# Performance work log

Measured on AMD Instinct MI355X. Metric: run time of the kernel, lower is better.

Reference implementation:

```python
import jax, jax.numpy as jnp
import numpy as np

N_NODES = 100000


def setup_inputs() -> dict:
    key = jax.random.key(0)
    ks = jax.random.split(key, 7)
    feats = jax.random.normal(ks[0], (N_NODES, 128), dtype=jnp.float32)
    src = jax.random.randint(ks[1], (1000000,), 0, N_NODES)
    dst = jax.random.randint(ks[2], (1000000,), 0, N_NODES)
    W1 = jax.random.normal(ks[3], (128, 128), dtype=jnp.float32) * (1.0 / np.sqrt(128))
    b1 = jnp.zeros((128,), dtype=jnp.float32)
    W2 = jax.random.normal(ks[4], (128, 40), dtype=jnp.float32) * (1.0 / np.sqrt(128))
    b2 = jnp.zeros((40,), dtype=jnp.float32)
    return {"feats": feats, "src": src, "dst": dst, "W1": W1, "b1": b1, "W2": W2, "b2": b2}


def _sage_gcn_layer(h, src, dst, deg, W, b):
    # DGL SAGEConv aggregator_type='gcn':
    #   neigh = sum over in-edges of src features; h = (neigh + h_self) / (in_deg + 1); out = h @ W + b
    neigh = jax.ops.segment_sum(h[src], dst, num_segments=N_NODES)  # [N, d]
    agg = (neigh + h) / (deg[:, None] + 1.0)
    return agg @ W + b


def reference(feats, src, dst, W1, b1, W2, b2):
    deg = jax.ops.segment_sum(jnp.ones_like(dst, dtype=feats.dtype), dst, num_segments=N_NODES)
    h1 = jax.nn.relu(_sage_gcn_layer(feats, src, dst, deg, W1, b1))  # dropout = identity (eval)
    h2 = _sage_gcn_layer(h1, src, dst, deg, W2, b2)
    # original returns (h_list, h); h_list = [h1, h2], final h = h2
    return (h1, h2)
```

## Files before the change

### kernel.cpp

```cpp
#include <hip/hip_runtime.h>

static inline int ceil_div(int a, int b){ return (a+b-1)/b; }

__global__ __launch_bounds__(256) void k_hist(const int* __restrict__ dst, int E, int* __restrict__ cnt){
  int e = blockIdx.x*256 + threadIdx.x;
  if (e < E) atomicAdd(&cnt[dst[e]], 1);
}

__global__ __launch_bounds__(256) void k_scan_a(const int* __restrict__ cnt, int N, int* __restrict__ bsum){
  __shared__ int s[256];
  int t = threadIdx.x;
  int i0 = blockIdx.x*512 + 2*t;
  int a = (i0   < N) ? cnt[i0]   : 0;
  int b = (i0+1 < N) ? cnt[i0+1] : 0;
  s[t] = a + b;
  __syncthreads();
  for (int off=128; off>0; off>>=1){ if (t<off) s[t]+=s[t+off]; __syncthreads(); }
  if (t==0) bsum[blockIdx.x] = s[0];
}

__global__ __launch_bounds__(256) void k_scan_b(int* __restrict__ bsum, int nb){
  __shared__ int s[256];
  int t = threadIdx.x;
  int v0=0,v1=0,v2=0,v3=0;
  int i0 = t*4;
  if (i0   < nb) v0 = bsum[i0];
  if (i0+1 < nb) v1 = bsum[i0+1];
  if (i0+2 < nb) v2 = bsum[i0+2];
  if (i0+3 < nb) v3 = bsum[i0+3];
  int tsum = v0+v1+v2+v3;
  s[t] = tsum;
  __syncthreads();
  for (int off=1; off<256; off<<=1){
    int v = (t>=off) ? s[t-off] : 0;
    __syncthreads();
    s[t] += v;
    __syncthreads();
  }
  int excl = s[t] - tsum;
  if (i0   < nb) bsum[i0]   = excl;
  if (i0+1 < nb) bsum[i0+1] = excl + v0;
  if (i0+2 < nb) bsum[i0+2] = excl + v0 + v1;
  if (i0+3 < nb) bsum[i0+3] = excl + v0 + v1 + v2;
}

__global__ __launch_bounds__(256) void k_scan_c(const int* __restrict__ cnt, int N,
                                                const int* __restrict__ bsum, int* __restrict__ offs){
  __shared__ int s[256];
  int t = threadIdx.x;
  int i0 = blockIdx.x*512 + 2*t;
  int a = (i0   < N) ? cnt[i0]   : 0;
  int b = (i0+1 < N) ? cnt[i0+1] : 0;
  int tsum = a+b;
  s[t] = tsum;
  __syncthreads();
  for (int off=1; off<256; off<<=1){
    int v = (t>=off) ? s[t-off] : 0;
    __syncthreads();
    s[t] += v;
    __syncthreads();
  }
  int excl = s[t] - tsum + bsum[blockIdx.x];
  if (i0   < N) offs[i0]   = excl;
  if (i0+1 < N) offs[i0+1] = excl + a;
}

__global__ __launch_bounds__(256) void k_place(const int* __restrict__ src, const int* __restrict__ dst, int E,
                                               int* __restrict__ offs, int* __restrict__ ss){
  int e = blockIdx.x*256 + threadIdx.x;
  if (e < E){
    int d = dst[e];
    int p = atomicAdd(&offs[d], 1);
    ss[p] = src[e];
  }
}

__global__ __launch_bounds__(256) void k_fused1(const float* __restrict__ feats,
    const int* __restrict__ ss, const int* __restrict__ offs, const int* __restrict__ cnt,
    const float* __restrict__ W1, const float* __restrict__ b1,
    const float* __restrict__ W2,
    float* __restrict__ h1, float* __restrict__ t1, int N){
  __shared__ float sA[64*132];
  __shared__ float sW[40*132];
  int t = threadIdx.x;
  int r0 = blockIdx.x*64;

  {
    int wid = t >> 6, lane = t & 63;
    const float2* f2 = (const float2*)feats;
    for (int k2=0; k2<16; ++k2){
      int rr = wid*16 + k2;
      int w  = r0 + rr;
      float2 acc = make_float2(0.f, 0.f);
      if (w < N){
        int c   = __builtin_amdgcn_readfirstlane(cnt[w]);
        int beg = __builtin_amdgcn_readfirstlane(offs[w]) - c;
        acc = f2[(size_t)w*64 + lane];
        int i = 0;
        for (; i+8 <= c; i += 8){
          int s0=ss[beg+i  ], s1=ss[beg+i+1], s2=ss[beg+i+2], s3=ss[beg+i+3];
          int s4=ss[beg+i+4], s5=ss[beg+i+5], s6=ss[beg+i+6], s7=ss[beg+i+7];
          float2 a0=f2[(size_t)s0*64+lane], a1=f2[(size_t)s1*64+lane];
          float2 a2=f2[(size_t)s2*64+lane], a3=f2[(size_t)s3*64+lane];
          float2 a4=f2[(size_t)s4*64+lane], a5=f2[(size_t)s5*64+lane];
          float2 a6=f2[(size_t)s6*64+lane], a7=f2[(size_t)s7*64+lane];
          acc.x += ((a0.x+a1.x)+(a2.x+a3.x)) + ((a4.x+a5.x)+(a6.x+a7.x));
          acc.y += ((a0.y+a1.y)+(a2.y+a3.y)) + ((a4.y+a5.y)+(a6.y+a7.y));
        }
        for (; i < c; ++i){
          int s0 = ss[beg+i];
          float2 a = f2[(size_t)s0*64 + lane];
          acc.x += a.x; acc.y += a.y;
        }
        float inv = 1.0f / (float)(c + 1);
        acc.x *= inv; acc.y *= inv;
      }
      *(float2*)&sA[rr*132 + 2*lane] = acc;
    }
  }

  int rg = t>>4, cg = t&15;
  float acc[4][8];
#pragma unroll
  for (int i=0;i<4;++i)
#pragma unroll
    for (int j=0;j<8;++j) acc[i][j]=0.f;

  for (int kc=0; kc<4; ++kc){
    __syncthreads();
#pragma unroll
    for (int it=0; it<4; ++it){
      int flat = it*1024 + t*4;
      *(float4*)&sW[flat] = *(const float4*)(W1 + kc*4096 + flat);
    }
    __syncthreads();
#pragma unroll 4
    for (int dd=0; dd<32; ++dd){
      int d = kc*32 + dd;
      float4 w0 = *(const float4*)&sW[dd*128 + cg*4];
      float4 w1 = *(const float4*)&sW[dd*128 + 64 + cg*4];
      float a0 = sA[(rg   )*132 + d];
      float a1 = sA[(rg+16)*132 + d];
      float a2 = sA[(rg+32)*132 + d];
      float a3 = sA[(rg+48)*132 + d];
      acc[0][0]+=a0*w0.x; acc[0][1]+=a0*w0.y; acc[0][2]+=a0*w0.z; acc[0][3]+=a0*w0.w;
      acc[0][4]+=a0*w1.x; acc[0][5]+=a0*w1.y; acc[0][6]+=a0*w1.z; acc[0][7]+=a0*w1.w;
      acc[1][0]+=a1*w0.x; acc[1][1]+=a1*w0.y; acc[1][2]+=a1*w0.z; acc[1][3]+=a1*w0.w;
      acc[1][4]+=a1*w1.x; acc[1][5]+=a1*w1.y; acc[1][6]+=a1*w1.z; acc[1][7]+=a1*w1.w;
      acc[2][0]+=a2*w0.x; acc[2][1]+=a2*w0.y; acc[2][2]+=a2*w0.z; acc[2][3]+=a2*w0.w;
      acc[2][4]+=a2*w1.x; acc[2][5]+=a2*w1.y; acc[2][6]+=a2*w1.z; acc[2][7]+=a2*w1.w;
      acc[3][0]+=a3*w0.x; acc[3][1]+=a3*w0.y; acc[3][2]+=a3*w0.z; acc[3][3]+=a3*w0.w;
      acc[3][4]+=a3*w1.x; acc[3][5]+=a3*w1.y; acc[3][6]+=a3*w1.z; acc[3][7]+=a3*w1.w;
    }
  }
  __syncthreads();

  float4 bb0 = *(const float4*)(b1 + cg*4);
  float4 bb1 = *(const float4*)(b1 + 64 + cg*4);
#pragma unroll
  for (int i=0;i<4;++i){
    int rr = rg + i*16;
    int r  = r0 + rr;
    float4 o0, o1;
    o0.x = fmaxf(acc[i][0]+bb0.x, 0.f); o0.y = fmaxf(acc[i][1]+bb0.y, 0.f);
    o0.z = fmaxf(acc[i][2]+bb0.z, 0.f); o0.w = fmaxf(acc[i][3]+bb0.w, 0.f);
    o1.x = fmaxf(acc[i][4]+bb1.x, 0.f); o1.y = fmaxf(acc[i][5]+bb1.y, 0.f);
    o1.z = fmaxf(acc[i][6]+bb1.z, 0.f); o1.w = fmaxf(acc[i][7]+bb1.w, 0.f);
    *(float4*)&sA[rr*132 + cg*4]      = o0;
    *(float4*)&sA[rr*132 + 64 + cg*4] = o1;
    if (r < N){
      *(float4*)(h1 + (size_t)r*128 + cg*4)      = o0;
      *(float4*)(h1 + (size_t)r*128 + 64 + cg*4) = o1;
    }
  }
#pragma unroll
  for (int it=0; it<5; ++it){
    int flat = it*1024 + t*4;
    float4 v = *(const float4*)(W2 + flat);
    const float* vp = (const float*)&v;
#pragma unroll
    for (int j=0;j<4;++j){
      int idx = flat + j;
      int d = idx / 40, col = idx % 40;
      sW[col*132 + d] = vp[j];
    }
  }
  __syncthreads();

  int rg2 = t>>3, cg2 = t&7;
  float a2c[2][5];
#pragma unroll
  for (int i=0;i<2;++i)
#pragma unroll
    for (int j=0;j<5;++j) a2c[i][j]=0.f;
  for (int d0=0; d0<32; ++d0){
    float4 a0 = *(const float4*)&sA[(rg2   )*132 + 4*d0];
    float4 a1 = *(const float4*)&sA[(rg2+32)*132 + 4*d0];
#pragma unroll
    for (int jj=0;jj<5;++jj){
      float4 wv = *(const float4*)&sW[(cg2+8*jj)*132 + 4*d0];
      a2c[0][jj] += a0.x*wv.x + a0.y*wv.y + a0.z*wv.z + a0.w*wv.w;
      a2c[1][jj] += a1.x*wv.x + a1.y*wv.y + a1.z*wv.z + a1.w*wv.w;
    }
  }
#pragma unroll
  for (int i=0;i<2;++i){
    int r = r0 + rg2 + i*32;
    if (r < N){
#pragma unroll
      for (int jj=0;jj<5;++jj) t1[(size_t)r*40 + cg2 + 8*jj] = a2c[i][jj];
    }
  }
}

__global__ __launch_bounds__(256) void k_agg2(const float* __restrict__ t1,
    const int* __restrict__ ss, const int* __restrict__ offs, const int* __restrict__ cnt,
    const float* __restrict__ b2, float* __restrict__ h2, int N){
  int w = (int)((blockIdx.x*256u + threadIdx.x) >> 6);
  int lane = threadIdx.x & 63;
  if (w >= N) return;
  int c   = __builtin_amdgcn_readfirstlane(cnt[w]);
  int beg = __builtin_amdgcn_readfirstlane(offs[w]) - c;
  int l = (lane < 40) ? lane : 0;
  float acc = t1[(size_t)w*40 + l];
  int i = 0;
  for (; i+4 <= c; i += 4){
    int s0 = ss[beg+i], s1 = ss[beg+i+1], s2 = ss[beg+i+2], s3 = ss[beg+i+3];
    float a = t1[(size_t)s0*40 + l];
    float b = t1[(size_t)s1*40 + l];
    float cc= t1[(size_t)s2*40 + l];
    float d = t1[(size_t)s3*40 + l];
    acc += (a + b) + (cc + d);
  }
  for (; i < c; ++i) acc += t1[(size_t)ss[beg+i]*40 + l];
  float inv = 1.0f / (float)(c + 1);
  if (lane < 40) h2[(size_t)w*40 + lane] = acc*inv + b2[lane];
}

extern "C" void kernel_launch(void* const* d_in, const int* in_sizes, int n_in,
                              void* d_out, int out_size, void* d_ws, size_t ws_size,
                              hipStream_t stream){
  const float* feats = (const float*)d_in[0];
  const int*   src   = (const int*)d_in[1];
  const int*   dst   = (const int*)d_in[2];
  const float* W1    = (const float*)d_in[3];
  const float* b1    = (const float*)d_in[4];
  const float* W2    = (const float*)d_in[5];
  const float* b2    = (const float*)d_in[6];
  int N = in_sizes[0] / 128;
  int E = in_sizes[1];
  float* h1 = (float*)d_out;
  float* h2 = h1 + (size_t)N*128;

  size_t need = 0;
  auto lay = [&](size_t bytes)->size_t{ size_t p = need; need += (bytes + 511) & ~(size_t)511; return p; };
  size_t o_cnt    = lay((size_t)N*4);
  size_t o_offs   = lay((size_t)N*4);
  size_t o_bsum   = lay(4096);
  size_t o_ss     = lay((size_t)E*4);
  size_t o_t1     = lay((size_t)N*40*4);
  if (need > ws_size) return;

  char* wp = (char*)d_ws;
  int*   cnt    = (int*)(wp + o_cnt);
  int*   offs   = (int*)(wp + o_offs);
  int*   bsum   = (int*)(wp + o_bsum);
  int*   ss     = (int*)(wp + o_ss);
  float* t1     = (float*)(wp + o_t1);

  hipMemsetAsync(cnt, 0, (size_t)N*4, stream);

  int nb = ceil_div(N, 512);
  k_hist  <<<ceil_div(E,256), 256, 0, stream>>>(dst, E, cnt);
  k_scan_a<<<nb,              256, 0, stream>>>(cnt, N, bsum);
  k_scan_b<<<1,               256, 0, stream>>>(bsum, nb);
  k_scan_c<<<nb,              256, 0, stream>>>(cnt, N, bsum, offs);
  k_place <<<ceil_div(E,256), 256, 0, stream>>>(src, dst, E, offs, ss);

  k_fused1<<<ceil_div(N,64),  256, 0, stream>>>(feats, ss, offs, cnt, W1, b1, W2, h1, t1, N);
  k_agg2  <<<ceil_div(N,4),   256, 0, stream>>>(t1, ss, offs, cnt, b2, h2, N);
}
```

Measured before the change: 465.4 us.

## Split layer-1 aggregation into its own wave-per-node kernel, staging through h1

Layer-1 neighbor aggregation moves out of the fused GEMM kernel into a separate kernel that gives each node one wavefront and launches many more blocks. It writes the aggregated features into the h1 buffer, which the GEMM kernel then reads back and overwrites in place. The point is to get more latency hiding for the random gathers than the old 64-row blocks with 16 serial rows per wave could offer. The GEMM inner loops also switch to float4 LDS reads of A. The cost is an extra write and read of a 100000x128 float intermediate, plus one more kernel launch.

```diff
diff --git a/kernel.cpp b/kernel.cpp
--- a/kernel.cpp
+++ b/kernel.cpp
@@ -75,50 +75,50 @@
   }
 }
 
-__global__ __launch_bounds__(256) void k_fused1(const float* __restrict__ feats,
+__global__ __launch_bounds__(256) void k_agg1(const float* __restrict__ feats,
     const int* __restrict__ ss, const int* __restrict__ offs, const int* __restrict__ cnt,
+    float* __restrict__ aggout, int N){
+  int w = (int)((blockIdx.x*256u + threadIdx.x) >> 6);
+  int lane = threadIdx.x & 63;
+  if (w >= N) return;
+  int c   = __builtin_amdgcn_readfirstlane(cnt[w]);
+  int beg = __builtin_amdgcn_readfirstlane(offs[w]) - c;
+  const float2* f2 = (const float2*)feats;
+  float2 acc = f2[(size_t)w*64 + lane];
+  int i = 0;
+  for (; i+4 <= c; i += 4){
+    int s0 = ss[beg+i], s1 = ss[beg+i+1], s2 = ss[beg+i+2], s3 = ss[beg+i+3];
+    float2 a = f2[(size_t)s0*64 + lane];
+    float2 b = f2[(size_t)s1*64 + lane];
+    float2 cc= f2[(size_t)s2*64 + lane];
+    float2 d = f2[(size_t)s3*64 + lane];
+    acc.x += (a.x + b.x) + (cc.x + d.x);
+    acc.y += (a.y + b.y) + (cc.y + d.y);
+  }
+  for (; i < c; ++i){
+    int s0 = ss[beg+i];
+    float2 a = f2[(size_t)s0*64 + lane];
+    acc.x += a.x; acc.y += a.y;
+  }
+  float inv = 1.0f / (float)(c + 1);
+  float2 o; o.x = acc.x*inv; o.y = acc.y*inv;
+  ((float2*)aggout)[(size_t)w*64 + lane] = o;
+}
+
+__global__ __launch_bounds__(256) void k_gemm12(float* __restrict__ h1,
     const float* __restrict__ W1, const float* __restrict__ b1,
-    const float* __restrict__ W2,
-    float* __restrict__ h1, float* __restrict__ t1, int N){
+    const float* __restrict__ W2, float* __restrict__ t1, int N){
   __shared__ float sA[64*132];
-  __shared__ float sW[40*132];
+  __shared__ float sW[5280];
   int t = threadIdx.x;
   int r0 = blockIdx.x*64;
-
-  {
-    int wid = t >> 6, lane = t & 63;
-    const float2* f2 = (const float2*)feats;
-    for (int k2=0; k2<16; ++k2){
-      int rr = wid*16 + k2;
-      int w  = r0 + rr;
-      float2 acc = make_float2(0.f, 0.f);
-      if (w < N){
-        int c   = __builtin_amdgcn_readfirstlane(cnt[w]);
-        int beg = __builtin_amdgcn_readfirstlane(offs[w]) - c;
-        acc = f2[(size_t)w*64 + lane];
-        int i = 0;
-        for (; i+8 <= c; i += 8){
-          int s0=ss[beg+i  ], s1=ss[beg+i+1], s2=ss[beg+i+2], s3=ss[beg+i+3];
-          int s4=ss[beg+i+4], s5=ss[beg+i+5], s6=ss[beg+i+6], s7=ss[beg+i+7];
-          float2 a0=f2[(size_t)s0*64+lane], a1=f2[(size_t)s1*64+lane];
-          float2 a2=f2[(size_t)s2*64+lane], a3=f2[(size_t)s3*64+lane];
-          float2 a4=f2[(size_t)s4*64+lane], a5=f2[(size_t)s5*64+lane];
-          float2 a6=f2[(size_t)s6*64+lane], a7=f2[(size_t)s7*64+lane];
-          acc.x += ((a0.x+a1.x)+(a2.x+a3.x)) + ((a4.x+a5.x)+(a6.x+a7.x));
-          acc.y += ((a0.y+a1.y)+(a2.y+a3.y)) + ((a4.y+a5.y)+(a6.y+a7.y));
-        }
-        for (; i < c; ++i){
-          int s0 = ss[beg+i];
-          float2 a = f2[(size_t)s0*64 + lane];
-          acc.x += a.x; acc.y += a.y;
-        }
-        float inv = 1.0f / (float)(c + 1);
-        acc.x *= inv; acc.y *= inv;
-      }
-      *(float2*)&sA[rr*132 + 2*lane] = acc;
-    }
-  }
-
+  for (int it=0; it<8; ++it){
+    int flat = it*1024 + t*4;
+    int r = flat>>7, d = flat&127;
+    float4 v = make_float4(0.f,0.f,0.f,0.f);
+    if (r0+r < N) v = *(const float4*)(h1 + (size_t)(r0+r)*128 + d);
+    *(float4*)&sA[r*132 + d] = v;
+  }
   int rg = t>>4, cg = t&15;
   float acc[4][8];
 #pragma unroll
@@ -134,23 +134,35 @@
       *(float4*)&sW[flat] = *(const float4*)(W1 + kc*4096 + flat);
     }
     __syncthreads();
-#pragma unroll 4
-    for (int dd=0; dd<32; ++dd){
-      int d = kc*32 + dd;
-      float4 w0 = *(const float4*)&sW[dd*128 + cg*4];
-      float4 w1 = *(const float4*)&sW[dd*128 + 64 + cg*4];
-      float a0 = sA[(rg   )*132 + d];
-      float a1 = sA[(rg+16)*132 + d];
-      float a2 = sA[(rg+32)*132 + d];
-      float a3 = sA[(rg+48)*132 + d];
-      acc[0][0]+=a0*w0.x; acc[0][1]+=a0*w0.y; acc[0][2]+=a0*w0.z; acc[0][3]+=a0*w0.w;
-      acc[0][4]+=a0*w1.x; acc[0][5]+=a0*w1.y; acc[0][6]+=a0*w1.z; acc[0][7]+=a0*w1.w;
-      acc[1][0]+=a1*w0.x; acc[1][1]+=a1*w0.y; acc[1][2]+=a1*w0.z; acc[1][3]+=a1*w0.w;
-      acc[1][4]+=a1*w1.x; acc[1][5]+=a1*w1.y; acc[1][6]+=a1*w1.z; acc[1][7]+=a1*w1.w;
-      acc[2][0]+=a2*w0.x; acc[2][1]+=a2*w0.y; acc[2][2]+=a2*w0.z; acc[2][3]+=a2*w0.w;
-      acc[2][4]+=a2*w1.x; acc[2][5]+=a2*w1.y; acc[2][6]+=a2*w1.z; acc[2][7]+=a2*w1.w;
-      acc[3][0]+=a3*w0.x; acc[3][1]+=a3*w0.y; acc[3][2]+=a3*w0.z; acc[3][3]+=a3*w0.w;
-      acc[3][4]+=a3*w1.x; acc[3][5]+=a3*w1.y; acc[3][6]+=a3*w1.z; acc[3][7]+=a3*w1.w;
+    const float* a0p = &sA[(rg   )*132 + kc*32];
+    const float* a1p = &sA[(rg+16)*132 + kc*32];
+    const float* a2p = &sA[(rg+32)*132 + kc*32];
+    const float* a3p = &sA[(rg+48)*132 + kc*32];
+    const float* wp  = &sW[cg*4];
+#pragma unroll
+    for (int dq=0; dq<8; ++dq){
+      float4 a0 = *(const float4*)(a0p + dq*4);
+      float4 a1 = *(const float4*)(a1p + dq*4);
+      float4 a2 = *(const float4*)(a2p + dq*4);
+      float4 a3 = *(const float4*)(a3p + dq*4);
+      const float* a0f = (const float*)&a0;
+      const float* a1f = (const float*)&a1;
+      const float* a2f = (const float*)&a2;
+      const float* a3f = (const float*)&a3;
+#pragma unroll
+      for (int j=0; j<4; ++j){
+        float4 w0 = *(const float4*)(wp + (dq*4+j)*128);
+        float4 w1 = *(const float4*)(wp + (dq*4+j)*128 + 64);
+        float v0 = a0f[j], v1 = a1f[j], v2 = a2f[j], v3 = a3f[j];
+        acc[0][0]+=v0*w0.x; acc[0][1]+=v0*w0.y; acc[0][2]+=v0*w0.z; acc[0][3]+=v0*w0.w;
+        acc[0][4]+=v0*w1.x; acc[0][5]+=v0*w1.y; acc[0][6]+=v0*w1.z; acc[0][7]+=v0*w1.w;
+        acc[1][0]+=v1*w0.x; acc[1][1]+=v1*w0.y; acc[1][2]+=v1*w0.z; acc[1][3]+=v1*w0.w;
+        acc[1][4]+=v1*w1.x; acc[1][5]+=v1*w1.y; acc[1][6]+=v1*w1.z; acc[1][7]+=v1*w1.w;
+        acc[2][0]+=v2*w0.x; acc[2][1]+=v2*w0.y; acc[2][2]+=v2*w0.z; acc[2][3]+=v2*w0.w;
+        acc[2][4]+=v2*w1.x; acc[2][5]+=v2*w1.y; acc[2][6]+=v2*w1.z; acc[2][7]+=v2*w1.w;
+        acc[3][0]+=v3*w0.x; acc[3][1]+=v3*w0.y; acc[3][2]+=v3*w0.z; acc[3][3]+=v3*w0.w;
+        acc[3][4]+=v3*w1.x; acc[3][5]+=v3*w1.y; acc[3][6]+=v3*w1.z; acc[3][7]+=v3*w1.w;
+      }
     }
   }
   __syncthreads();
@@ -193,14 +205,33 @@
   for (int i=0;i<2;++i)
 #pragma unroll
     for (int j=0;j<5;++j) a2c[i][j]=0.f;
-  for (int d0=0; d0<32; ++d0){
-    float4 a0 = *(const float4*)&sA[(rg2   )*132 + 4*d0];
-    float4 a1 = *(const float4*)&sA[(rg2+32)*132 + 4*d0];
-#pragma unroll
-    for (int jj=0;jj<5;++jj){
-      float4 wv = *(const float4*)&sW[(cg2+8*jj)*132 + 4*d0];
-      a2c[0][jj] += a0.x*wv.x + a0.y*wv.y + a0.z*wv.z + a0.w*wv.w;
-      a2c[1][jj] += a1.x*wv.x + a1.y*wv.y + a1.z*wv.z + a1.w*wv.w;
+  {
+    const float* aB0 = &sA[(rg2   )*132];
+    const float* aB1 = &sA[(rg2+32)*132];
+    const float* wB0 = &sW[(cg2     )*132];
+    const float* wB1 = &sW[(cg2+ 8)*132];
+    const float* wB2 = &sW[(cg2+16)*132];
+    const float* wB3 = &sW[(cg2+24)*132];
+    const float* wB4 = &sW[(cg2+32)*132];
+#pragma unroll 8
+    for (int d0=0; d0<32; ++d0){
+      float4 a0 = *(const float4*)(aB0 + 4*d0);
+      float4 a1 = *(const float4*)(aB1 + 4*d0);
+      float4 w0 = *(const float4*)(wB0 + 4*d0);
+      float4 w1 = *(const float4*)(wB1 + 4*d0);
+      float4 w2 = *(const float4*)(wB2 + 4*d0);
+      float4 w3 = *(const float4*)(wB3 + 4*d0);
+      float4 w4 = *(const float4*)(wB4 + 4*d0);
+      a2c[0][0] += a0.x*w0.x + a0.y*w0.y + a0.z*w0.z + a0.w*w0.w;
+      a2c[0][1] += a0.x*w1.x + a0.y*w1.y + a0.z*w1.z + a0.w*w1.w;
+      a2c[0][2] += a0.x*w2.x + a0.y*w2.y + a0.z*w2.z + a0.w*w2.w;
+      a2c[0][3] += a0.x*w3.x + a0.y*w3.y + a0.z*w3.z + a0.w*w3.w;
+      a2c[0][4] += a0.x*w4.x + a0.y*w4.y + a0.z*w4.z + a0.w*w4.w;
+      a2c[1][0] += a1.x*w0.x + a1.y*w0.y + a1.z*w0.z + a1.w*w0.w;
+      a2c[1][1] += a1.x*w1.x + a1.y*w1.y + a1.z*w1.z + a1.w*w1.w;
+      a2c[1][2] += a1.x*w2.x + a1.y*w2.y + a1.z*w2.z + a1.w*w2.w;
+      a2c[1][3] += a1.x*w3.x + a1.y*w3.y + a1.z*w3.z + a1.w*w3.w;
+      a2c[1][4] += a1.x*w4.x + a1.y*w4.y + a1.z*w4.z + a1.w*w4.w;
     }
   }
 #pragma unroll
@@ -277,6 +308,7 @@
   k_scan_c<<<nb,              256, 0, stream>>>(cnt, N, bsum, offs);
   k_place <<<ceil_div(E,256), 256, 0, stream>>>(src, dst, E, offs, ss);
 
-  k_fused1<<<ceil_div(N,64),  256, 0, stream>>>(feats, ss, offs, cnt, W1, b1, W2, h1, t1, N);
+  k_agg1  <<<ceil_div(N,4),   256, 0, stream>>>(feats, ss, offs, cnt, h1, N);
+  k_gemm12<<<ceil_div(N,64),  256, 0, stream>>>(h1, W1, b1, W2, t1, N);
   k_agg2  <<<ceil_div(N,4),   256, 0, stream>>>(t1, ss, offs, cnt, b2, h2, N);
 }
```

After: 447.8 us. 3.8% less time.
